# Performance work log

Hardware: AMD Instinct MI355X
Metric: run time of the kernel (lower is better)

Reference implementation:

```python
import jax, jax.numpy as jnp
import numpy as np
import math

B, T, TE, D, H = 1, 2048, 1024, 1024, 16
HD = D // H
INF = 1e9  # infinity_proxy from the original module
INIT_SCALE = 0.02


def sinusoid_pos_emb(timesteps, dim):
    # Transformer-XL sinusoids for relative positions [timesteps-1 .. 0].
    inv_freq = 1.0 / (10000.0 ** (np.arange(0, dim, 2) / dim))
    pos_seq = np.arange(timesteps - 1, -1, -1.0)
    inp = np.einsum('i,j->ij', pos_seq, inv_freq)
    return np.concatenate([np.sin(inp), np.cos(inp)], axis=-1).astype(np.float32)


def relative_shift(x):
    # x: [b, h, t, T] -> TXL left-pad / reshape / slice shift trick.
    b, h, t1, t2 = x.shape
    x = jnp.pad(x, ((0, 0), (0, 0), (0, 0), (1, 0)))
    x = x.reshape(b, h, t2 + 1, t1)[:, :, 1:, :]
    return x.reshape(b, h, t1, t2)


def setup_inputs() -> dict:
    key = jax.random.key(0)
    ks = jax.random.split(key, 12)
    s = INIT_SCALE
    x = jax.random.normal(ks[0], (B, T, D), jnp.float32)
    extra = jax.random.normal(ks[1], (B, TE, D), jnp.float32)
    # causal mask over the in-sequence keys; full visibility on the extra memory
    mask = jnp.broadcast_to(jnp.tril(jnp.ones((T, T), jnp.float32))[None, None], (B, 1, T, T))
    extra_mask = jnp.ones((B, 1, T, TE), jnp.float32)
    Wq = jax.random.normal(ks[2], (D, D), jnp.float32) * s
    Wk = jax.random.normal(ks[3], (D, D), jnp.float32) * s
    Wv = jax.random.normal(ks[4], (D, D), jnp.float32) * s
    Wek = jax.random.normal(ks[5], (D, D), jnp.float32) * s
    Wev = jax.random.normal(ks[6], (D, D), jnp.float32) * s
    Wr = jax.random.normal(ks[7], (D, D), jnp.float32) * s
    Wo = jax.random.normal(ks[8], (D, D), jnp.float32) * s
    r_w_bias = jax.random.normal(ks[9], (H, HD), jnp.float32) * s
    r_r_bias = jax.random.normal(ks[10], (H, HD), jnp.float32) * s
    return dict(x=x, extra=extra, mask=mask, extra_mask=extra_mask,
                Wq=Wq, Wk=Wk, Wv=Wv, Wek=Wek, Wev=Wev, Wr=Wr, Wo=Wo,
                r_w_bias=r_w_bias, r_r_bias=r_r_bias)


def reference(x, extra, mask, extra_mask, Wq, Wk, Wv, Wek, Wev, Wr, Wo, r_w_bias, r_r_bias):
    b, t, d = x.shape
    te = extra.shape[1]
    # conv1d(kernel=1, no bias) == matmul projections; cache_steps=0 so y == x
    q = (x @ Wq).reshape(b, t, H, HD)
    k = (x @ Wk).reshape(b, t, H, HD)
    v = (x @ Wv).reshape(b, t, H, HD)
    # Transformer-XL relative-position attend_fn
    pos = jnp.asarray(sinusoid_pos_emb(t, d))            # [t, D]
    r = (pos @ Wr).reshape(t, H, HD)                      # [t, H, HD]
    content = jnp.einsum('bthd,bThd->bhtT', q + r_w_bias, k)
    rel = relative_shift(jnp.einsum('bthd,Thd->bhtT', q + r_r_bias, r))
    attn = content + rel
    attn = attn * mask - INF * (1.0 - mask)
    # extra keys/values use plain dot-product attention (no rel-pos)
    ek = (extra @ Wek).reshape(b, te, H, HD)
    ev = (extra @ Wev).reshape(b, te, H, HD)
    eattn = jnp.einsum('bthd,bThd->bhtT', q, ek)
    eattn = eattn * extra_mask - INF * (1.0 - extra_mask)
    attn = jnp.concatenate([attn, eattn], axis=-1) * (1.0 / math.sqrt(HD))
    p = jax.nn.softmax(attn, axis=-1)
    vv = jnp.concatenate([v, ev], axis=1)                 # [b, t+te, H, HD]
    out = jnp.einsum('bhtT,bThd->bthd', p, vv).reshape(b, t, d)
    return out @ Wo  # final conv1d, with_final_bias=False
```

## Files before the change

kernel.cpp:

```cpp
#include <hip/hip_runtime.h>
#include <hip/hip_bf16.h>
#include <math.h>

#define T_LEN 2048
#define TE_LEN 1024
#define D_DIM 1024
#define H_NUM 16
#define HD_DIM 64
#define R_PAD 64

typedef unsigned short ushort;
typedef __attribute__((ext_vector_type(8))) short short8;
typedef __attribute__((ext_vector_type(4))) float f32x4;
typedef __attribute__((ext_vector_type(4))) ushort ushort4v;

__device__ __forceinline__ ushort f2b(float f) {
    unsigned u = __builtin_bit_cast(unsigned, f);
    u += 0x7fffu + ((u >> 16) & 1u);
    return (ushort)(u >> 16);
}
__device__ __forceinline__ float b2f(ushort s) {
    unsigned u = ((unsigned)s) << 16;
    return __builtin_bit_cast(float, u);
}

__device__ __forceinline__ void gld16(const ushort* g, ushort* l) {
    __builtin_amdgcn_global_load_lds(
        (const __attribute__((address_space(1))) unsigned int*)g,
        (__attribute__((address_space(3))) unsigned int*)l, 16, 0, 0);
}

union U8 { short8 v; ushort u[8]; };

__global__ void prep_kernel(const float* __restrict__ x, const float* __restrict__ extra,
                            ushort* __restrict__ pos, ushort* __restrict__ xb,
                            ushort* __restrict__ eb) {
    const int q = blockIdx.x * 256 + threadIdx.x;
    const int PQ = 524288;
    const int XQ = 1048576;
    if (q < PQ) {
        int idx = q * 4;
        int i = idx >> 10, j = idx & 1023;
        bool sinreg = (j < 512);
        int jj = sinreg ? j : j - 512;
        float p = (float)(2047 - i);
        ushort4v o;
#pragma unroll
        for (int u = 0; u < 4; u++) {
            float inv = exp2f((float)(jj + u) * -0.025952563241f);
            float fa = p * inv;
            ((ushort*)&o)[u] = f2b(sinreg ? sinf(fa) : cosf(fa));
        }
        *(ushort4v*)&pos[idx] = o;
    } else if (q < XQ) {
        int idx = (q - PQ) * 4;
        float4 v = *(const float4*)&x[idx];
        ushort4v o = {f2b(v.x), f2b(v.y), f2b(v.z), f2b(v.w)};
        *(ushort4v*)&xb[idx] = o;
    } else {
        int idx = (q - XQ) * 4;
        float4 v = *(const float4*)&extra[idx];
        ushort4v o = {f2b(v.x), f2b(v.y), f2b(v.z), f2b(v.w)};
        *(ushort4v*)&eb[idx] = o;
    }
}

__global__ __launch_bounds__(256) void transpose7_kernel(
    const float* __restrict__ W0, const float* __restrict__ W1,
    const float* __restrict__ W2, const float* __restrict__ W3,
    const float* __restrict__ W4, const float* __restrict__ W5,
    const float* __restrict__ W6, ushort* __restrict__ out,
    ushort* __restrict__ Rpad) {
    if (blockIdx.z == 7) {
        int gid = (blockIdx.y * 32 + blockIdx.x) * 256 + threadIdx.x;
        if (gid < (R_PAD * 1024) / 8) {
            short8 z = {0, 0, 0, 0, 0, 0, 0, 0};
            *(short8*)&Rpad[gid * 8] = z;
        }
        return;
    }
    const float* Ws[7] = {W0, W1, W2, W3, W4, W5, W6};
    const float* W = Ws[blockIdx.z];
    ushort* WT = out + (size_t)blockIdx.z * (1024 * 1024);
    __shared__ float tile[32][33];
    int c0 = blockIdx.x * 32, r0 = blockIdx.y * 32;
    int tid = threadIdx.x;
#pragma unroll
    for (int p = 0; p < 4; p++) {
        int idx = tid + p * 256;
        int r = idx >> 5, c = idx & 31;
        tile[r][c] = W[(size_t)(r0 + r) * D_DIM + c0 + c];
    }
    __syncthreads();
#pragma unroll
    for (int p = 0; p < 4; p++) {
        int idx = tid + p * 256;
        int r = idx >> 5, c = idx & 31;
        WT[(size_t)(c0 + r) * D_DIM + r0 + c] = f2b(tile[c][r]);
    }
}

__global__ __launch_bounds__(256) void gemm_mega(
    const ushort* __restrict__ xb, const ushort* __restrict__ posb,
    const ushort* __restrict__ eb, const ushort* __restrict__ WT,
    ushort* __restrict__ Qb, ushort* __restrict__ Kb, ushort* __restrict__ VTb,
    ushort* __restrict__ Rb, ushort* __restrict__ EKb, ushort* __restrict__ EVTb) {
    __shared__ ushort As[128 * 64];
    __shared__ ushort Bs[128 * 64];
    const int tid = threadIdx.x;
    const int lane = tid & 63, w = tid >> 6;
    const int l15 = lane & 15, quad = lane >> 4;
    const int wm = w & 1, wn = w >> 1;
    const size_t M1 = 1024 * 1024;

    int idx = blockIdx.x;
    const ushort *A, *BT;
    ushort* dst;
    int m0, nb0, nc0, ldt = 1024;
    bool transp = false;
    if (idx < 384) {
        m0 = (idx & 15) * 128; nb0 = (idx >> 4) * 128;
        A = xb; BT = WT;
        nc0 = nb0 & 1023;
        int seg = nb0 >> 10;
        if (seg == 0) dst = Qb;
        else if (seg == 1) dst = Kb;
        else { dst = VTb; transp = true; ldt = T_LEN; }
    } else if (idx < 512) {
        int i = idx - 384;
        m0 = (i & 15) * 128; nb0 = (i >> 4) * 128; nc0 = nb0;
        A = posb; BT = WT + 5 * M1; dst = Rb;
    } else {
        int i = idx - 512;
        m0 = (i & 7) * 128; nb0 = (i >> 3) * 128; nc0 = nb0 & 1023;
        A = eb; BT = WT + 3 * M1;
        if (nb0 < 1024) dst = EKb;
        else { dst = EVTb; transp = true; ldt = TE_LEN; }
    }

    f32x4 acc[16];
#pragma unroll
    for (int i = 0; i < 16; i++) acc[i] = (f32x4){0.f, 0.f, 0.f, 0.f};

    for (int k0 = 0; k0 < 1024; k0 += 64) {
        __syncthreads();
#pragma unroll
        for (int i = 0; i < 4; i++) {
            int ci = i * 256 + tid;
            int row = ci >> 3, cs = (ci & 7) ^ (row & 7);
            gld16(A + (size_t)(m0 + row) * 1024 + k0 + cs * 8, &As[(i * 32 + w * 8) * 64]);
            gld16(BT + (size_t)(nb0 + row) * 1024 + k0 + cs * 8, &Bs[(i * 32 + w * 8) * 64]);
        }
        __syncthreads();
#pragma unroll
        for (int kc = 0; kc < 2; kc++) {
            short8 bfr[4];
#pragma unroll
            for (int nf = 0; nf < 4; nf++) {
                const int row = wn * 64 + nf * 16 + l15;
                bfr[nf] = *(const short8*)&Bs[(row * 8 + ((kc * 4 + quad) ^ (row & 7))) * 8];
            }
#pragma unroll
            for (int mf = 0; mf < 4; mf++) {
                const int row = wm * 64 + mf * 16 + l15;
                short8 afr = *(const short8*)&As[(row * 8 + ((kc * 4 + quad) ^ (row & 7))) * 8];
#pragma unroll
                for (int nf = 0; nf < 4; nf++)
                    acc[mf * 4 + nf] = __builtin_amdgcn_mfma_f32_16x16x32_bf16(afr, bfr[nf], acc[mf * 4 + nf], 0, 0, 0);
            }
        }
    }

#pragma unroll
    for (int mf = 0; mf < 4; mf++) {
#pragma unroll
        for (int nf = 0; nf < 4; nf++) {
            f32x4 a = acc[mf * 4 + nf];
            const int mrow = m0 + wm * 64 + mf * 16 + quad * 4;
            const int nc = nc0 + wn * 64 + nf * 16 + l15;
            if (transp) {
                ushort4v v = {f2b(a[0]), f2b(a[1]), f2b(a[2]), f2b(a[3])};
                *(ushort4v*)&dst[(size_t)nc * ldt + mrow] = v;
            } else {
#pragma unroll
                for (int r = 0; r < 4; r++) dst[(size_t)(mrow + r) * 1024 + nc] = f2b(a[r]);
            }
        }
    }
}

__global__ __launch_bounds__(256) void gemm_wo(const ushort* __restrict__ A,
                                               const ushort* __restrict__ BT,
                                               float* __restrict__ out) {
    __shared__ ushort As[128 * 64];
    __shared__ ushort Bs[64 * 64];
    const int tid = threadIdx.x;
    const int lane = tid & 63, w = tid >> 6;
    const int l15 = lane & 15, quad = lane >> 4;
    const int wm = w & 1, wn = w >> 1;
    const int m0 = blockIdx.y * 128, n0 = blockIdx.x * 64;

    f32x4 acc[8];
#pragma unroll
    for (int i = 0; i < 8; i++) acc[i] = (f32x4){0.f, 0.f, 0.f, 0.f};

    for (int k0 = 0; k0 < 1024; k0 += 64) {
        __syncthreads();
#pragma unroll
        for (int i = 0; i < 4; i++) {
            int ci = i * 256 + tid;
            int row = ci >> 3, cs = (ci & 7) ^ (row & 7);
            gld16(A + (size_t)(m0 + row) * 1024 + k0 + cs * 8, &As[(i * 32 + w * 8) * 64]);
        }
#pragma unroll
        for (int i = 0; i < 2; i++) {
            int ci = i * 256 + tid;
            int row = ci >> 3, cs = (ci & 7) ^ (row & 7);
            gld16(BT + (size_t)(n0 + row) * 1024 + k0 + cs * 8, &Bs[(i * 32 + w * 8) * 64]);
        }
        __syncthreads();
#pragma unroll
        for (int kc = 0; kc < 2; kc++) {
            short8 bfr[2];
#pragma unroll
            for (int nf = 0; nf < 2; nf++) {
                const int row = wn * 32 + nf * 16 + l15;
                bfr[nf] = *(const short8*)&Bs[(row * 8 + ((kc * 4 + quad) ^ (row & 7))) * 8];
            }
#pragma unroll
            for (int mf = 0; mf < 4; mf++) {
                const int row = wm * 64 + mf * 16 + l15;
                short8 afr = *(const short8*)&As[(row * 8 + ((kc * 4 + quad) ^ (row & 7))) * 8];
#pragma unroll
                for (int nf = 0; nf < 2; nf++)
                    acc[mf * 2 + nf] = __builtin_amdgcn_mfma_f32_16x16x32_bf16(afr, bfr[nf], acc[mf * 2 + nf], 0, 0, 0);
            }
        }
    }

#pragma unroll
    for (int mf = 0; mf < 4; mf++) {
#pragma unroll
        for (int nf = 0; nf < 2; nf++) {
            f32x4 a = acc[mf * 2 + nf];
            const int mrow = m0 + wm * 64 + mf * 16 + quad * 4;
            const int nc = n0 + wn * 32 + nf * 16 + l15;
#pragma unroll
            for (int r = 0; r < 4; r++) out[(size_t)(mrow + r) * 1024 + nc] = a[r];
        }
    }
}

__global__ __launch_bounds__(512, 4) void attn_kernel(
    const ushort* __restrict__ Qb, const ushort* __restrict__ Kb,
    const ushort* __restrict__ VT, const ushort* __restrict__ Rb,
    const ushort* __restrict__ EKb, const ushort* __restrict__ EVT,
    const float* __restrict__ rwb, const float* __restrict__ rrb,
    ushort* __restrict__ AOb) {
    __shared__ __align__(16) ushort lds[21504];

    const int tid = threadIdx.x;
    const int lane = tid & 63, w = tid >> 6;
    const int g = w >> 2, wl = w & 3;
    const int gtid = tid & 255;
    const int l15 = lane & 15, quad = lane >> 4;
    const int blk = blockIdx.x;
    const int xcd = blk & 7, rnd = blk >> 8, slot = (blk >> 3) & 31;
    const int h = xcd * 2 + rnd;
    const int qt = rnd ? slot : 31 - slot;
    const int t0 = qt * 64, tf = t0 + wl * 16;
    const int hbase = h * HD_DIM;
    const int base0 = 1984 - t0;
    const int ninl = qt + 1;
    const int ntotl = ninl + 16;
    const int tt_s = g * ninl;
    const int baseg = base0 + 32 * tt_s;

    ushort* Kst = lds + g * 4096;
    ushort* Vst = lds + 8192 + g * 4096;
    ushort* Pw  = lds + 16384 + w * 640;

    short8 qw[2], qr[2], qp[2];
#pragma unroll
    for (int kh = 0; kh < 2; kh++) {
        int dof = hbase + kh * 32 + quad * 8;
        U8 raw; raw.v = *(const short8*)&Qb[(size_t)(tf + l15) * D_DIM + dof];
        U8 a, b, c;
#pragma unroll
        for (int j = 0; j < 8; j++) {
            float f = b2f(raw.u[j]);
            a.u[j] = f2b((f + rwb[dof + j]) * 0.125f);
            b.u[j] = f2b((f + rrb[dof + j]) * 0.125f);
            c.u[j] = f2b(f * 0.125f);
        }
        qw[kh] = a.v; qr[kh] = b.v; qp[kh] = c.v;
    }

    float lr[4] = {0.f, 0.f, 0.f, 0.f};
    f32x4 O[4];
#pragma unroll
    for (int i = 0; i < 4; i++) O[i] = (f32x4){0.f, 0.f, 0.f, 0.f};
    f32x4 rel_carry = (f32x4){0.f, 0.f, 0.f, 0.f};

    auto stageKV = [&](int i2, int buf) {
        const bool ins = i2 < ninl;
        const int j0 = ins ? (tt_s + i2) * 32 : (g * 16 + (i2 - ninl)) * 32;
        const ushort* ksrc = ins ? Kb : EKb;
        const ushort* vsrc = ins ? VT : EVT;
        const int ldv = ins ? T_LEN : TE_LEN;
        {
            int row = gtid >> 3, cs = (gtid & 7) ^ (row & 7);
            gld16(ksrc + (size_t)(j0 + row) * 1024 + hbase + cs * 8,
                  &Kst[buf * 2048 + wl * 512]);
        }
        {
            int row = gtid >> 2, cs = (gtid & 3) ^ (row & 3);
            gld16(vsrc + (size_t)(hbase + row) * ldv + j0 + cs * 8,
                  &Vst[buf * 2048 + wl * 512]);
        }
    };

    stageKV(0, 0);

    int srcA[4]; bool lowcA[4];
#pragma unroll
    for (int r = 0; r < 4; r++) {
        const int m = quad * 4 + r;
        const int cb = 15 - m + l15;
        srcA[r] = (lane & 48) | (cb & 15);
        lowcA[r] = (cb < 16);
    }

#pragma unroll 1
    for (int i = 0; i < ntotl; i++) {
        const int b = i & 1;
        __syncthreads();
        if (i + 1 < ntotl) stageKV(i + 1, 1 - b);

        const bool ins = i < ninl;
        const int j0 = (tt_s + i) * 32;

        short8 rf1[2], rf2[2], rf0[2];
        if (ins) {
            const size_t rbase =
                (size_t)(baseg + 48 - 16 * wl + 32 * i + l15) * 1024 + hbase + quad * 8;
#pragma unroll
            for (int kh = 0; kh < 2; kh++) {
                rf1[kh] = *(const short8*)&Rb[rbase + 16 * 1024 + kh * 32];
                rf2[kh] = *(const short8*)&Rb[rbase + 32 * 1024 + kh * 32];
            }
            if (i == 0) {
#pragma unroll
                for (int kh = 0; kh < 2; kh++)
                    rf0[kh] = *(const short8*)&Rb[rbase + kh * 32];
            }
        }

        f32x4 con[2];
#pragma unroll
        for (int c = 0; c < 2; c++) con[c] = (f32x4){0.f, 0.f, 0.f, 0.f};
#pragma unroll
        for (int kh = 0; kh < 2; kh++) {
            const short8* qa = ins ? &qw[kh] : &qp[kh];
#pragma unroll
            for (int nh = 0; nh < 2; nh++) {
                const int row = nh * 16 + l15;
                short8 kf = *(const short8*)&Kst[b * 2048 + (row * 8 + ((kh * 4 + quad) ^ (row & 7))) * 8];
                con[nh] = __builtin_amdgcn_mfma_f32_16x16x32_bf16(*qa, kf, con[nh], 0, 0, 0);
            }
        }

        if (ins) {
            f32x4 relA, rel1, rel2;
            rel1 = (f32x4){0.f, 0.f, 0.f, 0.f};
            rel2 = (f32x4){0.f, 0.f, 0.f, 0.f};
            if (i == 0) {
                relA = (f32x4){0.f, 0.f, 0.f, 0.f};
#pragma unroll
                for (int kh = 0; kh < 2; kh++)
                    relA = __builtin_amdgcn_mfma_f32_16x16x32_bf16(qr[kh], rf0[kh], relA, 0, 0, 0);
            } else {
                relA = rel_carry;
            }
#pragma unroll
            for (int kh = 0; kh < 2; kh++) {
                rel1 = __builtin_amdgcn_mfma_f32_16x16x32_bf16(qr[kh], rf1[kh], rel1, 0, 0, 0);
                rel2 = __builtin_amdgcn_mfma_f32_16x16x32_bf16(qr[kh], rf2[kh], rel2, 0, 0, 0);
            }
            rel_carry = rel2;

            const bool needmask = (j0 + 31 > tf);
#pragma unroll
            for (int r = 0; r < 4; r++) {
                const int m = quad * 4 + r;
                float b0 = __shfl(relA[r], srcA[r]);
                float b1 = __shfl(rel1[r], srcA[r]);
                float b2 = __shfl(rel2[r], srcA[r]);
                float rv0 = lowcA[r] ? b0 : b1, rv1 = lowcA[r] ? b1 : b2;
                float p0 = __expf(con[0][r] + rv0);
                float p1 = __expf(con[1][r] + rv1);
                if (needmask) {
                    const int t = tf + m;
                    if (j0 + l15 > t)      p0 = 0.f;
                    if (j0 + 16 + l15 > t) p1 = 0.f;
                }
                lr[r] += p0 + p1;
                Pw[m * 40 + l15]      = f2b(p0);
                Pw[m * 40 + 16 + l15] = f2b(p1);
            }
        } else {
#pragma unroll
            for (int r = 0; r < 4; r++) {
                const int m = quad * 4 + r;
                float p0 = __expf(con[0][r]);
                float p1 = __expf(con[1][r]);
                lr[r] += p0 + p1;
                Pw[m * 40 + l15]      = f2b(p0);
                Pw[m * 40 + 16 + l15] = f2b(p1);
            }
        }

        short8 pa = *(const short8*)&Pw[l15 * 40 + quad * 8];
#pragma unroll
        for (int df = 0; df < 4; df++) {
            const int row = df * 16 + l15;
            short8 vb = *(const short8*)&Vst[b * 2048 + (row * 4 + (quad ^ (row & 3))) * 8];
            O[df] = __builtin_amdgcn_mfma_f32_16x16x32_bf16(pa, vb, O[df], 0, 0, 0);
        }
    }

#pragma unroll
    for (int r = 0; r < 4; r++)
#pragma unroll
        for (int dd = 1; dd < 16; dd <<= 1) lr[r] += __shfl_xor(lr[r], dd);

    float* exch = (float*)(lds);
    float* exl  = (float*)(lds + 12288);
    __syncthreads();
    if (g == 1) {
#pragma unroll
        for (int r = 0; r < 4; r++) {
            const int row = wl * 16 + quad * 4 + r;
            if (l15 == 0) exl[row] = lr[r];
#pragma unroll
            for (int df = 0; df < 4; df++)
                exch[row * 65 + df * 16 + l15] = O[df][r];
        }
    }
    __syncthreads();
    if (g == 0) {
#pragma unroll
        for (int r = 0; r < 4; r++) {
            const int row = wl * 16 + quad * 4 + r;
            const float inv = 1.0f / (lr[r] + exl[row]);
#pragma unroll
            for (int df = 0; df < 4; df++)
                AOb[(size_t)(t0 + row) * D_DIM + hbase + df * 16 + l15] =
                    f2b((O[df][r] + exch[row * 65 + df * 16 + l15]) * inv);
        }
    }
}

extern "C" void kernel_launch(void* const* d_in, const int* in_sizes, int n_in,
                              void* d_out, int out_size, void* d_ws, size_t ws_size,
                              hipStream_t stream) {
    const float* x     = (const float*)d_in[0];
    const float* extra = (const float*)d_in[1];
    const float* Wq  = (const float*)d_in[4];
    const float* Wk  = (const float*)d_in[5];
    const float* Wv  = (const float*)d_in[6];
    const float* Wek = (const float*)d_in[7];
    const float* Wev = (const float*)d_in[8];
    const float* Wr  = (const float*)d_in[9];
    const float* Wo  = (const float*)d_in[10];
    const float* rwb = (const float*)d_in[11];
    const float* rrb = (const float*)d_in[12];
    float* out = (float*)d_out;

    ushort* ws = (ushort*)d_ws;
    const size_t M1 = 1024 * 1024;
    size_t o = 0;
    ushort* posb = ws + o; o += 2 * M1;
    ushort* xb   = ws + o; o += 2 * M1;
    ushort* eb   = ws + o; o += M1;
    ushort* WT   = ws + o; o += 7 * M1;
    ushort* Qb   = ws + o; o += 2 * M1;
    ushort* Kb   = ws + o; o += 2 * M1;
    ushort* VTb  = ws + o; o += 2 * M1;
    ushort* Rb   = ws + o; o += (size_t)(T_LEN + R_PAD) * 1024;
    ushort* EKb  = ws + o; o += M1;
    ushort* EVTb = ws + o; o += M1;
    ushort* AOb  = posb;

    prep_kernel<<<5120, 256, 0, stream>>>(x, extra, posb, xb, eb);
    transpose7_kernel<<<dim3(32, 32, 8), 256, 0, stream>>>(
        Wq, Wk, Wv, Wek, Wev, Wr, Wo, WT, Rb + (size_t)T_LEN * 1024);

    gemm_mega<<<640, 256, 0, stream>>>(xb, posb, eb, WT, Qb, Kb, VTb, Rb, EKb, EVTb);

    attn_kernel<<<512, 512, 0, stream>>>(Qb, Kb, VTb, Rb, EKb, EVTb, rwb, rrb, AOb);

    gemm_wo<<<dim3(16, 16), 256, 0, stream>>>(AOb, WT + 6 * M1, out);
}
```

Before: 297.7 us.

## Stage relative-position R rows through an LDS ring buffer in attention kernel

Relative-position embedding rows are now loaded asynchronously into a 96-row LDS ring buffer, prefetched alongside K/V tiles, instead of being read directly from global memory each iteration. The P scratch tile is also compacted to a 32-wide XOR-swizzled layout to avoid bank conflicts. The change targets global-load latency on the R operand. In exchange it raises LDS use to 64KB per block, drops the occupancy hint from launch bounds, and adds an extra barrier in iterations where R is restaged, which may lower occupancy.

```diff
diff --git a/kernel.cpp b/kernel.cpp
--- a/kernel.cpp
+++ b/kernel.cpp
@@ -251,13 +251,13 @@
     }
 }
 
-__global__ __launch_bounds__(512, 4) void attn_kernel(
+__global__ __launch_bounds__(512) void attn_kernel(
     const ushort* __restrict__ Qb, const ushort* __restrict__ Kb,
     const ushort* __restrict__ VT, const ushort* __restrict__ Rb,
     const ushort* __restrict__ EKb, const ushort* __restrict__ EVT,
     const float* __restrict__ rwb, const float* __restrict__ rrb,
     ushort* __restrict__ AOb) {
-    __shared__ __align__(16) ushort lds[21504];
+    __shared__ __align__(16) ushort lds[32768];
 
     const int tid = threadIdx.x;
     const int lane = tid & 63, w = tid >> 6;
@@ -265,9 +265,9 @@
     const int gtid = tid & 255;
     const int l15 = lane & 15, quad = lane >> 4;
     const int blk = blockIdx.x;
-    const int xcd = blk & 7, rnd = blk >> 8, slot = (blk >> 3) & 31;
+    const int xcd = blk & 7, rnd = blk >> 8, qslot = (blk >> 3) & 31;
     const int h = xcd * 2 + rnd;
-    const int qt = rnd ? slot : 31 - slot;
+    const int qt = rnd ? qslot : 31 - qslot;
     const int t0 = qt * 64, tf = t0 + wl * 16;
     const int hbase = h * HD_DIM;
     const int base0 = 1984 - t0;
@@ -278,7 +278,8 @@
 
     ushort* Kst = lds + g * 4096;
     ushort* Vst = lds + 8192 + g * 4096;
-    ushort* Pw  = lds + 16384 + w * 640;
+    ushort* Rst = lds + 16384 + g * 6144;
+    ushort* Pw  = lds + 28672 + w * 512;
 
     short8 qw[2], qr[2], qp[2];
 #pragma unroll
@@ -319,7 +320,20 @@
                   &Vst[buf * 2048 + wl * 512]);
         }
     };
-
+    auto stageR = [&](int slotbase, int rowbase) {
+        int k = gtid >> 3;
+        int cs = (gtid & 7) ^ (k & 7);
+        gld16(Rb + (size_t)(rowbase + k) * 1024 + hbase + cs * 8,
+              &Rst[(slotbase + wl * 8) * 64]);
+    };
+
+#pragma unroll
+    for (int i = 0; i < 3; i++) {
+        int ci = i * 256 + gtid;
+        int k = ci >> 3, cs = (ci & 7) ^ (k & 7);
+        gld16(Rb + (size_t)(baseg + k) * 1024 + hbase + cs * 8,
+              &Rst[(i * 32 + wl * 8) * 64]);
+    }
     stageKV(0, 0);
 
     int srcA[4]; bool lowcA[4];
@@ -331,30 +345,43 @@
         lowcA[r] = (cb < 16);
     }
 
+    int sb = 0;
 #pragma unroll 1
     for (int i = 0; i < ntotl; i++) {
         const int b = i & 1;
         __syncthreads();
-        if (i + 1 < ntotl) stageKV(i + 1, 1 - b);
-
         const bool ins = i < ninl;
+        const bool stR = (i + 1 < ninl);
+
+        short8 rfa[2], rf1[2], rf2[2];
+        if (ins) {
+            const int key = l15 & 7;
+            const int o1 = 64 - 16 * wl + l15;
+            const int o2 = 80 - 16 * wl + l15;
+            int s1 = sb + o1; if (s1 >= 96) s1 -= 96;
+            int s2 = sb + o2; if (s2 >= 96) s2 -= 96;
+#pragma unroll
+            for (int kh = 0; kh < 2; kh++) {
+                rf1[kh] = *(const short8*)&Rst[(s1 * 8 + ((kh * 4 + quad) ^ key)) * 8];
+                rf2[kh] = *(const short8*)&Rst[(s2 * 8 + ((kh * 4 + quad) ^ key)) * 8];
+            }
+            if (i == 0) {
+                const int o0 = 48 - 16 * wl + l15;
+#pragma unroll
+                for (int kh = 0; kh < 2; kh++)
+                    rfa[kh] = *(const short8*)&Rst[(o0 * 8 + ((kh * 4 + quad) ^ key)) * 8];
+            }
+        }
+
+        if (stR) {
+            __syncthreads();
+            stageKV(i + 1, 1 - b);
+            stageR(sb, baseg + 96 + 32 * i);
+        } else if (i + 1 < ntotl) {
+            stageKV(i + 1, 1 - b);
+        }
+
         const int j0 = (tt_s + i) * 32;
-
-        short8 rf1[2], rf2[2], rf0[2];
-        if (ins) {
-            const size_t rbase =
-                (size_t)(baseg + 48 - 16 * wl + 32 * i + l15) * 1024 + hbase + quad * 8;
-#pragma unroll
-            for (int kh = 0; kh < 2; kh++) {
-                rf1[kh] = *(const short8*)&Rb[rbase + 16 * 1024 + kh * 32];
-                rf2[kh] = *(const short8*)&Rb[rbase + 32 * 1024 + kh * 32];
-            }
-            if (i == 0) {
-#pragma unroll
-                for (int kh = 0; kh < 2; kh++)
-                    rf0[kh] = *(const short8*)&Rb[rbase + kh * 32];
-            }
-        }
 
         f32x4 con[2];
 #pragma unroll
@@ -378,7 +405,7 @@
                 relA = (f32x4){0.f, 0.f, 0.f, 0.f};
 #pragma unroll
                 for (int kh = 0; kh < 2; kh++)
-                    relA = __builtin_amdgcn_mfma_f32_16x16x32_bf16(qr[kh], rf0[kh], relA, 0, 0, 0);
+                    relA = __builtin_amdgcn_mfma_f32_16x16x32_bf16(qr[kh], rfa[kh], relA, 0, 0, 0);
             } else {
                 relA = rel_carry;
             }
@@ -405,8 +432,9 @@
                     if (j0 + 16 + l15 > t) p1 = 0.f;
                 }
                 lr[r] += p0 + p1;
-                Pw[m * 40 + l15]      = f2b(p0);
-                Pw[m * 40 + 16 + l15] = f2b(p1);
+                const int sw = (r & 3) << 3;
+                Pw[m * 32 + (l15 ^ sw)]        = f2b(p0);
+                Pw[m * 32 + ((16 + l15) ^ sw)] = f2b(p1);
             }
         } else {
 #pragma unroll
@@ -415,18 +443,21 @@
                 float p0 = __expf(con[0][r]);
                 float p1 = __expf(con[1][r]);
                 lr[r] += p0 + p1;
-                Pw[m * 40 + l15]      = f2b(p0);
-                Pw[m * 40 + 16 + l15] = f2b(p1);
-            }
-        }
-
-        short8 pa = *(const short8*)&Pw[l15 * 40 + quad * 8];
+                const int sw = (r & 3) << 3;
+                Pw[m * 32 + (l15 ^ sw)]        = f2b(p0);
+                Pw[m * 32 + ((16 + l15) ^ sw)] = f2b(p1);
+            }
+        }
+
+        short8 pa = *(const short8*)&Pw[l15 * 32 + ((quad ^ (l15 & 3)) << 3)];
 #pragma unroll
         for (int df = 0; df < 4; df++) {
             const int row = df * 16 + l15;
             short8 vb = *(const short8*)&Vst[b * 2048 + (row * 4 + (quad ^ (row & 3))) * 8];
             O[df] = __builtin_amdgcn_mfma_f32_16x16x32_bf16(pa, vb, O[df], 0, 0, 0);
         }
+
+        sb += 32; if (sb >= 96) sb -= 96;
     }
 
 #pragma unroll
```

Measured after the change: 267.0 us. 1.12x faster.
